# Optimization experiments

Hardware: AMD Instinct MI355X
Metric: run time of the kernel (lower is better)

Reference implementation:

```python
import jax, jax.numpy as jnp
import numpy as np

N = 8192   # num_nodes
H = 128    # hidden_dim
B = 100    # batch of events
K = 5      # num_neg_samples
TD_MAX = 10000.0
TIME_SD = jnp.array([50.0, 7.0, 15.0, 15.0])  # time_sd from forward; time_mean = 0


def setup_inputs() -> dict:
    key = jax.random.key(0)
    ks = jax.random.split(key, 16)
    p = 32.0 / N  # avg degree ~32
    A = (jax.random.uniform(ks[0], (N, N)) < p).astype(jnp.float32)
    # S init: S[v,u] = 1/D[v] for neighbors u (row-normalized A)
    S = A / (A.sum(axis=1, keepdims=True) + 1e-7)
    z0 = jax.random.normal(ks[1], (N, H)) * 0.1
    u = jax.random.randint(ks[2], (B,), 0, N)
    v = jax.random.randint(ks[3], (B,), 0, N)
    event_types = jax.random.randint(ks[4], (B,), 0, 2)
    neg_idx = jax.random.randint(ks[5], (B, 2 * K), 0, N)
    time_diff = jax.random.normal(ks[6], (B, 2, 4))
    t_bar = jax.random.uniform(ks[7], (B, N)) * 1000.0
    t = 1000.0 + 10.0 * jnp.arange(B, dtype=jnp.float32)

    def lin(k, o, i):
        k1, k2 = jax.random.split(k)
        lim = 1.0 / np.sqrt(i)
        return (jax.random.uniform(k1, (o, i), minval=-lim, maxval=lim),
                jax.random.uniform(k2, (o,), minval=-lim, maxval=lim))

    om0_w, om0_b = lin(ks[8], 1, 2 * H)
    om1_w, om1_b = lin(ks[9], 1, 2 * H)
    Wh_w, Wh_b = lin(ks[10], H, H)
    Ws_w, Ws_b = lin(ks[11], H, H)
    Wr_w, Wr_b = lin(ks[12], H, H)
    Wt_w, Wt_b = lin(ks[13], H, 4)
    return dict(u=u, v=v, event_types=event_types, neg_idx=neg_idx,
                time_diff=time_diff, t_bar=t_bar, t=t, z0=z0, A=A, S=S,
                w_t=0.5 * jnp.ones(2), alpha=0.5 * jnp.ones(2), psi=0.5 * jnp.ones(2),
                om0_w=om0_w, om0_b=om0_b, om1_w=om1_w, om1_b=om1_b,
                Wh_w=Wh_w, Wh_b=Wh_b, Ws_w=Ws_w, Ws_b=Ws_b,
                Wr_w=Wr_w, Wr_b=Wr_b, Wt_w=Wt_w, Wt_b=Wt_b)


def _forward(u, v, event_types, neg_idx, time_diff, t_bar, t, z0, A, S,
             w_t, alpha, psi, om0_w, om0_b, om1_w, om1_b,
             Wh_w, Wh_b, Ws_w, Ws_b, Wr_w, Wr_b, Wt_w, Wt_b):
    td_norm = time_diff / TIME_SD  # (td - 0) / sd

    def hawkes(zu, zv, et, td):
        # lambda = psi * log(1 + exp(g/psi)) + alpha * exp(-w_t * td/td_max)
        zc = jnp.concatenate([zu, zv], axis=-1)
        g0 = jnp.einsum('...d,d->...', zc, om0_w[0]) + om0_b[0]
        g1 = jnp.einsum('...d,d->...', zc, om1_w[0]) + om1_b[0]
        g = jnp.where(et == 0, g0, g1)
        ps, al, wt = psi[et], alpha[et], w_t[et]
        gp = jnp.clip(g / (ps + 1e-7), -75.0, 75.0)
        return ps * jnp.log1p(jnp.exp(gp)) + al * jnp.exp(-wt * (td / TD_MAX))

    ar = jnp.arange(N)

    def step(z, ev):
        u_it, v_it, et, td2, tb, t_it, neg = ev
        z_u, z_v = z[u_it], z[v_it]
        Wh_all = z @ Wh_w.T + Wh_b  # [N,H]

        def struct(node):
            # structural attention over node's neighbors (masked, not dense loop)
            mask = A[node] > 0
            q = jnp.exp(S[node]) * mask
            q = q / (q.sum() + 1e-7)
            hsig = jax.nn.sigmoid(q[:, None] * Wh_all)
            hmax = jnp.where(mask[:, None], hsig, -jnp.inf).max(axis=0)
            return jnp.where(jnp.any(mask), hmax, 0.0)

        # update of u uses struct info from v's neighborhood, and vice versa
        hs = jnp.stack([struct(v_it), struct(u_it)])  # [2,H]
        h = (hs @ Ws_w.T + Ws_b) + (jnp.stack([z_u, z_v]) @ Wr_w.T + Wr_b) + (td2 @ Wt_w.T + Wt_b)
        z_upd = jax.nn.sigmoid(h)
        z_new = z.at[u_it].set(z_upd[0]).at[v_it].set(z_upd[1])

        # negative pairs: (u, v_neg_k) then (u_neg_k, v), using z_prev
        v_neg, u_neg = neg[:K], neg[K:]
        zu_neg = jnp.concatenate([jnp.broadcast_to(z_u, (K, H)), z[u_neg]], 0)
        zv_neg = jnp.concatenate([z[v_neg], jnp.broadcast_to(z_v, (K, H))], 0)
        lt_u = jnp.concatenate([jnp.full((K,), tb[u_it]), tb[u_neg]])
        lt_v = jnp.concatenate([tb[v_neg], jnp.full((K,), tb[v_it])])
        ts_neg = t_it - jnp.maximum(lt_u, lt_v)
        ts_pos = t_it - jnp.maximum(tb[u_it], tb[v_it])

        # all-node intensity prediction (Lambda_dict path, detached in torch)
        zd = jax.lax.stop_gradient(z)
        zu_all = jnp.concatenate([jnp.broadcast_to(jax.lax.stop_gradient(z_u), (N, H)),
                                  jnp.broadcast_to(jax.lax.stop_gradient(z_v), (N, H))], 0)
        zv_all = jnp.concatenate([zd, zd], 0)
        last_t = jnp.maximum(
            jnp.concatenate([jnp.full((N,), tb[u_it]), jnp.full((N,), tb[v_it])]),
            jnp.concatenate([tb, tb]))
        lam_all = hawkes(zu_all, zv_all, jnp.full((2 * N,), et),
                         jax.lax.stop_gradient(t_it - last_t))
        m = ((ar != u_it) & (ar != v_it)).astype(lam_all.dtype)
        lam_sum = jax.lax.stop_gradient(jnp.sum(lam_all * jnp.concatenate([m, m])))

        return z_new, (z_u, z_v, zu_neg, zv_neg, ts_pos, ts_neg, lam_sum)

    _, (zu_p, zv_p, zun, zvn, ts_p, ts_n, lam_sums) = jax.lax.scan(
        step, z0, (u, v, event_types, td_norm, t_bar, t, neg_idx))

    lam_pos = hawkes(zu_p, zv_p, event_types, ts_p)            # [B]
    lam_neg = hawkes(zun, zvn, event_types[:, None], ts_n)      # [B,2K]
    return jnp.concatenate([lam_pos[:, None], lam_neg, lam_sums[:, None]], axis=1)  # [B, 2K+2]


def reference(u, v, event_types, neg_idx, time_diff, t_bar, t, z0, A, S,
              w_t, alpha, psi, om0_w, om0_b, om1_w, om1_b,
              Wh_w, Wh_b, Ws_w, Ws_b, Wr_w, Wr_b, Wt_w, Wt_b):
    return _forward(u, v, event_types, neg_idx, time_diff, t_bar, t, z0, A, S,
                    w_t, alpha, psi, om0_w, om0_b, om1_w, om1_b,
                    Wh_w, Wh_b, Ws_w, Ws_b, Wr_w, Wr_b, Wt_w, Wt_b)
```

## Files before the change

### kernel.cpp

```cpp
#include <hip/hip_runtime.h>
#include <math.h>

#define N 8192
#define H 128
#define BB 100
#define KK 5
#define MAXN 256
#define TD_MAXF 10000.0f

#define OFF_WHALLV ((size_t)N * H)
#define OFF_ZVER (OFF_WHALLV + 2 * BB * H)

__global__ __launch_bounds__(256) void prep_all_kernel(
    const float* __restrict__ Wh, const float* __restrict__ Ws,
    const float* __restrict__ Wr, const float* __restrict__ om0,
    const float* __restrict__ om1, const float* __restrict__ z0,
    float* __restrict__ WhT, float* __restrict__ WsT, float* __restrict__ WrT,
    float* __restrict__ omP, unsigned* __restrict__ flags,
    float* __restrict__ dvec0) {
  const int B0 = H * H, B1 = 2 * H * H, B2 = 3 * H * H;
  const int B3 = B2 + 2 * H, B4 = B2 + 4 * H, B5 = B4 + 4 * BB + 4;
  int idx = blockIdx.x * 256 + threadIdx.x;
  if (idx < B0) {
    int d = idx >> 7, k = idx & (H - 1);
    WhT[k * H + d] = Wh[d * H + k];
  } else if (idx < B1) {
    int e = idx - B0;
    int d = e >> 7, k = e & (H - 1);
    WsT[k * H + d] = Ws[d * H + k];
  } else if (idx < B2) {
    int e = idx - B1;
    int d = e >> 7, k = e & (H - 1);
    WrT[k * H + d] = Wr[d * H + k];
  } else if (idx < B3) {
    int e = idx - B2;
    omP[e] = om0[e];
  } else if (idx < B4) {
    int e = idx - B3;
    omP[2 * H + e] = om1[e];
  } else if (idx < B5) {
    flags[idx - B4] = 0u;
  } else if (idx < B5 + N) {
    int j = idx - B5;
    const float4* zr = (const float4*)(z0 + (size_t)j * H);
    const float4* o0 = (const float4*)om0;
    const float4* o1 = (const float4*)om1;
    float a0 = 0, b0 = 0, a1 = 0, b1 = 0;
    for (int k = 0; k < H / 4; ++k) {
      float4 zv = zr[k];
      float4 l0 = o0[k], r0 = o0[k + H / 4];
      float4 l1 = o1[k], r1 = o1[k + H / 4];
      a0 += zv.x * l0.x + zv.y * l0.y + zv.z * l0.z + zv.w * l0.w;
      b0 += zv.x * r0.x + zv.y * r0.y + zv.z * r0.z + zv.w * r0.w;
      a1 += zv.x * l1.x + zv.y * l1.y + zv.z * l1.z + zv.w * l1.w;
      b1 += zv.x * r1.x + zv.y * r1.y + zv.z * r1.z + zv.w * r1.w;
    }
    dvec0[0 * N + j] = a0;
    dvec0[1 * N + j] = b0;
    dvec0[2 * N + j] = a1;
    dvec0[3 * N + j] = b1;
  }
}

__global__ __launch_bounds__(256) void build_kernel(
    const float* __restrict__ z0, const float* __restrict__ WhT,
    const float* __restrict__ Wh_b, float* __restrict__ whall,
    const int* __restrict__ u_, const int* __restrict__ v_,
    const float* __restrict__ A, const float* __restrict__ S,
    int* __restrict__ cnt, int* __restrict__ nidx, float* __restrict__ nes,
    float* __restrict__ qsum, int* __restrict__ woff, int* __restrict__ zsrc,
    unsigned* __restrict__ need) {
  const int blk = blockIdx.x;
  const int tid = threadIdx.x;
  __shared__ float zr2[2][H];
  __shared__ int cnts[256];
  __shared__ int excl[257];
  __shared__ float ssum[256];
  __shared__ int nidxL[MAXN];
  __shared__ int uL[BB], vL[BB];

  if (blk < N / 2) {
    int r = tid >> 7, d = tid & (H - 1);
    int row = blk * 2 + r;
    zr2[r][d] = z0[(size_t)row * H + d];
    __syncthreads();
    float acc = Wh_b[d];
#pragma unroll 8
    for (int k = 0; k < H; ++k) acc += zr2[r][k] * WhT[k * H + d];
    whall[(size_t)row * H + d] = acc;
    return;
  }

  const int l = blk - N / 2;
  const int b = l >> 1, r = l & 1;
  const int node = r ? u_[b] : v_[b];
  int c = 0;
  float local = 0.0f;
  for (int it = 0; it < N / 256; ++it) {
    int j = it * 256 + tid;
    if (A[(size_t)node * N + j] > 0.0f) {
      ++c;
      local += expf(S[(size_t)node * N + j]);
    }
  }
  cnts[tid] = c;
  ssum[tid] = local;
  __syncthreads();
  if (tid == 0) {
    int s = 0;
    for (int i = 0; i < 256; ++i) { excl[i] = s; s += cnts[i]; }
    excl[256] = s;
  }
  __syncthreads();
  int p = excl[tid];
  for (int it = 0; it < N / 256; ++it) {
    int j = it * 256 + tid;
    if (A[(size_t)node * N + j] > 0.0f) {
      if (p < MAXN) {
        nidx[l * MAXN + p] = j;
        nidxL[p] = j;
        nes[l * MAXN + p] = expf(S[(size_t)node * N + j]);
      }
      ++p;
    }
  }
  if (tid < BB) {
    uL[tid] = u_[tid];
    vL[tid] = v_[tid];
  }
  __syncthreads();
  for (int s = 128; s > 0; s >>= 1) {
    if (tid < s) ssum[tid] += ssum[tid + s];
    __syncthreads();
  }
  const int cM = min(excl[256], MAXN);
  if (tid == 0) {
    cnt[l] = cM;
    qsum[l] = ssum[0];
  }
  for (int i = tid; i < cM; i += 256) {
    int n = nidxL[i];
    int a = -1, row = 0;
    for (int s = b - 1; s >= 0; --s) {
      if (vL[s] == n) { a = s; row = 1; break; }
      if (uL[s] == n) { a = s; row = 0; break; }
    }
    int off;
    if (a < 0) {
      off = n * H;
    } else {
      off = (int)OFF_WHALLV + (2 * a + row) * H;
      atomicOr(&need[b * 4 + (a >> 5)], 1u << (a & 31));
    }
    woff[l * MAXN + i] = off;
  }
  if (r == 0 && tid >= 254) {
    int which = tid - 254;
    int nd = which ? vL[b] : uL[b];
    int a = -1, row = 0;
    for (int s = b - 1; s >= 0; --s) {
      if (vL[s] == nd) { a = s; row = 1; break; }
      if (uL[s] == nd) { a = s; row = 0; break; }
    }
    int sv = -1;
    if (a >= 0) {
      sv = 2 * a + row;
      atomicOr(&need[b * 4 + (a >> 5)], 1u << (a & 31));
    }
    zsrc[2 * b + which] = sv;
  }
}

__global__ __launch_bounds__(1024) void fused_kernel(
    const int* __restrict__ u_, const int* __restrict__ v_,
    const int* __restrict__ et_, const int* __restrict__ neg_,
    const float* __restrict__ time_diff, const float* __restrict__ t_bar,
    const float* __restrict__ tt, const float* __restrict__ z0,
    const float* __restrict__ WhT, const float* __restrict__ WsT,
    const float* __restrict__ WrT, const float* __restrict__ omP,
    const float* __restrict__ Wh_b, const float* __restrict__ Ws_b,
    const float* __restrict__ Wr_b, const float* __restrict__ Wt_w,
    const float* __restrict__ Wt_b, const float* __restrict__ w_t,
    const float* __restrict__ alpha, const float* __restrict__ psi,
    const float* __restrict__ om0_b, const float* __restrict__ om1_b,
    const float* __restrict__ wsf, float* __restrict__ zver,
    float* __restrict__ whallv, float* __restrict__ dlog,
    const float* __restrict__ qsum_, const int* __restrict__ cnt_,
    const float* __restrict__ nes_, const int* __restrict__ woff_,
    const int* __restrict__ zsrc_, const float* __restrict__ dvec0,
    const unsigned* __restrict__ need, unsigned* done,
    float* __restrict__ out) {
  const int blk = blockIdx.x;
  const int t = threadIdx.x;
  __shared__ float scratch[8][2][H];
  __shared__ float hsS[2][H];
  __shared__ float zrowS[2][H];
  __shared__ float zupdS[2][H];
  __shared__ float td2S[2][4];
  __shared__ int woffS[2][MAXN];
  __shared__ float nqS[2][MAXN];
  __shared__ int cntS[2];
  __shared__ int uvS[2];
  __shared__ float dR[N];
  __shared__ int uS[BB], vS[BB];
  __shared__ float red[1024];
  __shared__ float suS, svS;

  if (blk < BB) {
    const int b = blk;
    const int r = t >> 9;
    const int sub = (t >> 7) & 3;
    const int d = t & (H - 1);
    const int l = 2 * b + r;
    const int c = cnt_[l];
    const float iq = 1.0f / (qsum_[l] + 1e-7f);
    const int ks = t >> 7;
    const int k0 = ks * 16;

    if (t < 512) {
      int rr = t >> 8, i = t & 255;
      woffS[rr][i] = woff_[(2 * b + rr) * MAXN + i];
      nqS[rr][i] = nes_[(2 * b + rr) * MAXN + i];
    } else if (t < 520) {
      int i = t - 512;
      int cc = i & 3;
      float sd = (cc == 0) ? 50.0f : ((cc == 1) ? 7.0f : 15.0f);
      td2S[i >> 2][cc] = time_diff[b * 8 + i] / sd;
    } else if (t < 522) {
      cntS[t - 520] = cnt_[2 * b + (t - 520)];
    } else if (t == 522) {
      uvS[0] = u_[b];
    } else if (t == 523) {
      uvS[1] = v_[b];
    }
    float wsReg[16], wrReg[16], whReg[16];
#pragma unroll
    for (int kk = 0; kk < 16; ++kk) {
      wsReg[kk] = WsT[(k0 + kk) * H + d];
      wrReg[kk] = WrT[(k0 + kk) * H + d];
      whReg[kk] = WhT[(k0 + kk) * H + d];
    }
    float biasReg = 0.0f, whbReg = 0.0f;
    float4 wt4Reg = {0.0f, 0.0f, 0.0f, 0.0f};
    float zpre = 0.0f;
    int zs = -1;
    if (t < 256) {
      int dd = t & (H - 1);
      biasReg = Ws_b[dd] + Wr_b[dd] + Wt_b[dd];
      whbReg = Wh_b[dd];
      wt4Reg = ((const float4*)Wt_w)[dd];
      int rr = t >> 7;
      zs = zsrc_[2 * b + rr];
      if (zs < 0) {
        int nd = rr ? v_[b] : u_[b];
        zpre = z0[(size_t)nd * H + dd];
      }
    }
    float omA = 0.0f, omB = 0.0f;
    if (t >= 256 && t < 768) {
      int w = (t - 256) >> 6;
      int lane = t & 63;
      int which = w & 3;
      int wsel = which >> 1;
      int offo = (which & 1) * H;
      omA = omP[wsel * 2 * H + offo + lane];
      omB = omP[wsel * 2 * H + offo + 64 + lane];
    }
    __syncthreads();

    float mx = -INFINITY;
    for (int i = sub; i < c; i += 4) {
      int off = woffS[r][i];
      if (off < (int)OFF_WHALLV)
        mx = fmaxf(mx, nqS[r][i] * iq * wsf[(size_t)off + d]);
    }
    if (t == 0) {
      for (int w = 0; w < 4; ++w) {
        unsigned nw = need[b * 4 + w];
        if (!nw) continue;
        while ((__hip_atomic_load(&done[w], __ATOMIC_RELAXED,
                                  __HIP_MEMORY_SCOPE_AGENT) &
                nw) != nw)
          __builtin_amdgcn_s_sleep(1);
      }
      __threadfence();
    }
    __syncthreads();

    const int ub = uvS[0], vb = uvS[1];

    for (int i = sub; i < c; i += 4) {
      int off = woffS[r][i];
      if (off >= (int)OFF_WHALLV)
        mx = fmaxf(mx, nqS[r][i] * iq * wsf[(size_t)off + d]);
    }
    scratch[sub][r][d] = mx;
    if (t < 256) {
      int rr = t >> 7, dd = t & (H - 1);
      zrowS[rr][dd] = (zs < 0) ? zpre : wsf[OFF_ZVER + (size_t)zs * H + dd];
    }
    __syncthreads();

    if (t < 2 * H) {
      int rr = t >> 7, dd = t & (H - 1);
      float m = fmaxf(fmaxf(scratch[0][rr][dd], scratch[1][rr][dd]),
                      fmaxf(scratch[2][rr][dd], scratch[3][rr][dd]));
      hsS[rr][dd] = (cntS[rr] > 0) ? (1.0f / (1.0f + expf(-m))) : 0.0f;
    }
    __syncthreads();

    {
      float a0 = 0.0f, a1 = 0.0f;
#pragma unroll
      for (int kk = 0; kk < 16; ++kk) {
        int k = k0 + kk;
        a0 += hsS[0][k] * wsReg[kk] + zrowS[0][k] * wrReg[kk];
        a1 += hsS[1][k] * wsReg[kk] + zrowS[1][k] * wrReg[kk];
      }
      scratch[ks][0][d] = a0;
      scratch[ks][1][d] = a1;
    }
    __syncthreads();

    if (t < 2 * H) {
      int rr = t >> 7, dd = t & (H - 1);
      float acc = biasReg;
#pragma unroll
      for (int kx = 0; kx < 8; ++kx) acc += scratch[kx][rr][dd];
      acc += td2S[rr][0] * wt4Reg.x + td2S[rr][1] * wt4Reg.y +
             td2S[rr][2] * wt4Reg.z + td2S[rr][3] * wt4Reg.w;
      float zu = 1.0f / (1.0f + expf(-acc));
      zupdS[rr][dd] = zu;
      zver[(size_t)(2 * b + rr) * H + dd] = zu;
    }
    __syncthreads();

    {
      int r0 = (ub == vb) ? 1 : 0;
      float f0 = 0.0f, f1 = 0.0f;
#pragma unroll
      for (int kk = 0; kk < 16; ++kk) {
        int k = k0 + kk;
        f0 += zupdS[r0][k] * whReg[kk];
        f1 += zupdS[1][k] * whReg[kk];
      }
      scratch[ks][0][d] = f0;
      scratch[ks][1][d] = f1;
    }
    __syncthreads();

    if (t < 2 * H) {
      int rr = t >> 7, dd = t & (H - 1);
      float acc = whbReg;
#pragma unroll
      for (int kx = 0; kx < 8; ++kx) acc += scratch[kx][rr][dd];
      whallv[(size_t)(2 * b + rr) * H + dd] = acc;
    } else if (t < 768) {
      int w = (t - 256) >> 6;
      int lane = t & 63;
      int row = w >> 2;
      int which = w & 3;
      int rr = (row == 0 && ub == vb) ? 1 : row;
      float val = zupdS[rr][lane] * omA + zupdS[rr][64 + lane] * omB;
      for (int s = 32; s > 0; s >>= 1) val += __shfl_down(val, s);
      if (lane == 0) dlog[b * 8 + which * 2 + row] = val;
    }
    __syncthreads();

    if (t == 0) {
      __threadfence();
      atomicOr(&done[b >> 5], 1u << (b & 31));
    }
    return;
  }

  const int b = blk - BB;
  const int e = et_[b];
  const int ub = u_[b], vb = v_[b];
  const float ps = psi[e], al = alpha[e], wt = w_t[e];
  const float ob0 = om0_b[0], ob1 = om1_b[0];
  const float ob = e ? ob1 : ob0;
  const float tcur = tt[b];
  const float inv_ps = 1.0f / (ps + 1e-7f);
  const int whichR = 2 * e + 1;
  const int whichL = 2 * e;

  if (t < BB) {
    uS[t] = u_[t];
    vS[t] = v_[t];
  }
  {
    const float4* base = (const float4*)(dvec0 + (size_t)whichR * N);
    float4* dst = (float4*)dR;
    for (int i = t; i < N / 4; i += 1024) dst[i] = base[i];
  }
  if (t == 0) {
    for (int w = 0; w < 4; ++w) {
      int cb = b - 32 * w;
      unsigned nw =
          (cb >= 32) ? 0xffffffffu : (cb <= 0 ? 0u : ((1u << cb) - 1u));
      if (!nw) continue;
      while ((__hip_atomic_load(&done[w], __ATOMIC_RELAXED,
                                __HIP_MEMORY_SCOPE_AGENT) &
              nw) != nw)
        __builtin_amdgcn_s_sleep(1);
    }
    __threadfence();
  }
  __syncthreads();

  for (int i = t; i < b; i += 1024) {
    int ui = uS[i], vi = vS[i];
    bool u_over = (ui == vi);
    bool v_over = false;
    for (int j = i + 1; j < b; ++j) {
      int uj = uS[j], vj = vS[j];
      u_over = u_over || (uj == ui) || (vj == ui);
      v_over = v_over || (uj == vi) || (vj == vi);
    }
    if (!u_over) dR[ui] = dlog[i * 8 + whichR * 2 + 0];
    if (!v_over) dR[vi] = dlog[i * 8 + whichR * 2 + 1];
  }

  if (t < 13) {
    auto dpre = [&](int x, int which) -> float {
      for (int bp = b - 1; bp >= 0; --bp) {
        if (vS[bp] == x) return dlog[bp * 8 + which * 2 + 1];
        if (uS[bp] == x) return dlog[bp * 8 + which * 2 + 0];
      }
      return dvec0[(size_t)which * N + x];
    };
    if (t < 11) {
      int li, ri;
      float ltu, ltv;
      if (t == 0) {
        li = ub; ri = vb;
        ltu = t_bar[(size_t)b * N + ub];
        ltv = t_bar[(size_t)b * N + vb];
      } else if (t <= 5) {
        int vn = neg_[b * (2 * KK) + (t - 1)];
        li = ub; ri = vn;
        ltu = t_bar[(size_t)b * N + ub];
        ltv = t_bar[(size_t)b * N + vn];
      } else {
        int un = neg_[b * (2 * KK) + (t - 1)];
        li = un; ri = vb;
        ltu = t_bar[(size_t)b * N + un];
        ltv = t_bar[(size_t)b * N + vb];
      }
      float g = dpre(li, whichL) + dpre(ri, whichR) + ob;
      float gp = fminf(fmaxf(g * inv_ps, -75.0f), 75.0f);
      float ts = tcur - fmaxf(ltu, ltv);
      out[b * 12 + t] = ps * log1pf(expf(gp)) + al * expf(-wt * (ts / TD_MAXF));
    } else if (t == 11) {
      suS = dpre(ub, whichL);
    } else {
      svS = dpre(vb, whichL);
    }
  }
  __syncthreads();

  const float su = suS, sv = svS;
  const float tb_u = t_bar[(size_t)b * N + ub];
  const float tb_v = t_bar[(size_t)b * N + vb];
  const float4* tb4 = (const float4*)(t_bar + (size_t)b * N);
  const float4* dR4 = (const float4*)dR;
  float acc = 0.0f;
  for (int j4 = t; j4 < N / 4; j4 += 1024) {
    float4 dv = dR4[j4];
    float4 tb = tb4[j4];
    float de[4] = {dv.x, dv.y, dv.z, dv.w};
    float te[4] = {tb.x, tb.y, tb.z, tb.w};
#pragma unroll
    for (int ee = 0; ee < 4; ++ee) {
      int j = j4 * 4 + ee;
      if (j == ub || j == vb) continue;
      float dd = de[ee];
      float tbj = te[ee];
      float gu = su + dd + ob;
      float gv = sv + dd + ob;
      float gpu_ = fminf(fmaxf(gu * inv_ps, -75.0f), 75.0f);
      float gpv_ = fminf(fmaxf(gv * inv_ps, -75.0f), 75.0f);
      float spl = ps * (log1pf(expf(gpu_)) + log1pf(expf(gpv_)));
      float tdu = tcur - fmaxf(tb_u, tbj);
      float tdv = tcur - fmaxf(tb_v, tbj);
      float ex =
          al * (expf(-wt * (tdu / TD_MAXF)) + expf(-wt * (tdv / TD_MAXF)));
      acc += spl + ex;
    }
  }
  red[t] = acc;
  __syncthreads();
  for (int s = 512; s > 0; s >>= 1) {
    if (t < s) red[t] += red[t + s];
    __syncthreads();
  }
  if (t == 0) out[b * 12 + 11] = red[0];
}

extern "C" void kernel_launch(void* const* d_in, const int* in_sizes, int n_in,
                              void* d_out, int out_size, void* d_ws,
                              size_t ws_size, hipStream_t stream) {
  const int* u = (const int*)d_in[0];
  const int* v = (const int*)d_in[1];
  const int* et = (const int*)d_in[2];
  const int* neg = (const int*)d_in[3];
  const float* time_diff = (const float*)d_in[4];
  const float* t_bar = (const float*)d_in[5];
  const float* t = (const float*)d_in[6];
  const float* z0 = (const float*)d_in[7];
  const float* A = (const float*)d_in[8];
  const float* S = (const float*)d_in[9];
  const float* w_t = (const float*)d_in[10];
  const float* alpha = (const float*)d_in[11];
  const float* psi = (const float*)d_in[12];
  const float* om0_w = (const float*)d_in[13];
  const float* om0_b = (const float*)d_in[14];
  const float* om1_w = (const float*)d_in[15];
  const float* om1_b = (const float*)d_in[16];
  const float* Wh_w = (const float*)d_in[17];
  const float* Wh_b = (const float*)d_in[18];
  const float* Ws_w = (const float*)d_in[19];
  const float* Ws_b = (const float*)d_in[20];
  const float* Wr_w = (const float*)d_in[21];
  const float* Wr_b = (const float*)d_in[22];
  const float* Wt_w = (const float*)d_in[23];
  const float* Wt_b = (const float*)d_in[24];
  float* out = (float*)d_out;

  float* wsf = (float*)d_ws;
  float* whall = wsf;
  float* whallv = wsf + OFF_WHALLV;
  float* zver = wsf + OFF_ZVER;
  float* WhT = zver + 2 * BB * H;
  float* WsT = WhT + H * H;
  float* WrT = WsT + H * H;
  float* omP = WrT + H * H;
  float* dvec0 = omP + 4 * H;
  float* dlog = dvec0 + 4 * N;
  float* qsum = dlog + 8 * BB;
  int* cnt = (int*)(qsum + 2 * BB);
  int* nidx = cnt + 2 * BB;
  float* nes = (float*)(nidx + 2 * BB * MAXN);
  int* woff = (int*)(nes + 2 * BB * MAXN);
  int* zsrc = woff + 2 * BB * MAXN;
  unsigned* need = (unsigned*)(zsrc + 2 * BB);
  unsigned* done = need + 4 * BB;

  const int PREP_ELEMS = 3 * H * H + 4 * H + 4 * BB + 4 + N;
  prep_all_kernel<<<(PREP_ELEMS + 255) / 256, 256, 0, stream>>>(
      Wh_w, Ws_w, Wr_w, om0_w, om1_w, z0, WhT, WsT, WrT, omP, need, dvec0);
  build_kernel<<<N / 2 + 2 * BB, 256, 0, stream>>>(
      z0, WhT, Wh_b, whall, u, v, A, S, cnt, nidx, nes, qsum, woff, zsrc,
      need);
  fused_kernel<<<2 * BB, 1024, 0, stream>>>(
      u, v, et, neg, time_diff, t_bar, t, z0, WhT, WsT, WrT, omP, Wh_b, Ws_b,
      Wr_b, Wt_w, Wt_b, w_t, alpha, psi, om0_b, om1_b, wsf, zver, whallv,
      dlog, qsum, cnt, nes, woff, zsrc, dvec0, need, done, out);
}
```

Baseline: 606.1 us.

## Drop weight-transpose prep kernel, fold into build, factor exps in lambda-sum loop

Removes the separate prep kernel that transposed Wh/Ws/Wr and copied the omega vectors. The matvecs now read the original row-major weights with float4 loads, the dvec0 dot products become extra blocks of build_kernel, and the flag clearing becomes a hipMemsetAsync. The second pass over the adjacency row is replaced by a per-thread bitmask from the first pass, so A is not reloaded. The survival-sum loop is refactored so softplus and the time-decay exponentials are written as products of per-event constants and per-node exponentials. This cuts transcendental work per node but drops the ±75 clamp, which risks overflow or reduced accuracy.

```diff
diff --git a/kernel.cpp b/kernel.cpp
--- a/kernel.cpp
+++ b/kernel.cpp
@@ -11,37 +11,43 @@
 #define OFF_WHALLV ((size_t)N * H)
 #define OFF_ZVER (OFF_WHALLV + 2 * BB * H)
 
-__global__ __launch_bounds__(256) void prep_all_kernel(
-    const float* __restrict__ Wh, const float* __restrict__ Ws,
-    const float* __restrict__ Wr, const float* __restrict__ om0,
-    const float* __restrict__ om1, const float* __restrict__ z0,
-    float* __restrict__ WhT, float* __restrict__ WsT, float* __restrict__ WrT,
-    float* __restrict__ omP, unsigned* __restrict__ flags,
-    float* __restrict__ dvec0) {
-  const int B0 = H * H, B1 = 2 * H * H, B2 = 3 * H * H;
-  const int B3 = B2 + 2 * H, B4 = B2 + 4 * H, B5 = B4 + 4 * BB + 4;
-  int idx = blockIdx.x * 256 + threadIdx.x;
-  if (idx < B0) {
-    int d = idx >> 7, k = idx & (H - 1);
-    WhT[k * H + d] = Wh[d * H + k];
-  } else if (idx < B1) {
-    int e = idx - B0;
-    int d = e >> 7, k = e & (H - 1);
-    WsT[k * H + d] = Ws[d * H + k];
-  } else if (idx < B2) {
-    int e = idx - B1;
-    int d = e >> 7, k = e & (H - 1);
-    WrT[k * H + d] = Wr[d * H + k];
-  } else if (idx < B3) {
-    int e = idx - B2;
-    omP[e] = om0[e];
-  } else if (idx < B4) {
-    int e = idx - B3;
-    omP[2 * H + e] = om1[e];
-  } else if (idx < B5) {
-    flags[idx - B4] = 0u;
-  } else if (idx < B5 + N) {
-    int j = idx - B5;
+__global__ __launch_bounds__(256) void build_kernel(
+    const float* __restrict__ z0, const float* __restrict__ Wh,
+    const float* __restrict__ Wh_b, float* __restrict__ whall,
+    const int* __restrict__ u_, const int* __restrict__ v_,
+    const float* __restrict__ A, const float* __restrict__ S,
+    const float* __restrict__ om0, const float* __restrict__ om1,
+    float* __restrict__ dvec0, int* __restrict__ cnt, int* __restrict__ nidx,
+    float* __restrict__ nes, float* __restrict__ qsum, int* __restrict__ woff,
+    int* __restrict__ zsrc, unsigned* __restrict__ need) {
+  const int blk = blockIdx.x;
+  const int tid = threadIdx.x;
+  __shared__ float zr2[2][H];
+  __shared__ int cnts[256];
+  __shared__ int excl[257];
+  __shared__ float ssum[256];
+  __shared__ int nidxL[MAXN];
+  __shared__ int uL[BB], vL[BB];
+
+  if (blk < N / 2) {
+    int r = tid >> 7, d = tid & (H - 1);
+    int row = blk * 2 + r;
+    zr2[r][d] = z0[(size_t)row * H + d];
+    __syncthreads();
+    float acc = Wh_b[d];
+    const float4* w4 = (const float4*)(Wh + (size_t)d * H);
+    const float4* z4 = (const float4*)zr2[r];
+#pragma unroll 8
+    for (int k4 = 0; k4 < H / 4; ++k4) {
+      float4 wv = w4[k4];
+      float4 zv = z4[k4];
+      acc += zv.x * wv.x + zv.y * wv.y + zv.z * wv.z + zv.w * wv.w;
+    }
+    whall[(size_t)row * H + d] = acc;
+    return;
+  }
+  if (blk >= N / 2 + 2 * BB) {
+    int j = (blk - N / 2 - 2 * BB) * 256 + tid;
     const float4* zr = (const float4*)(z0 + (size_t)j * H);
     const float4* o0 = (const float4*)om0;
     const float4* o1 = (const float4*)om1;
@@ -59,35 +65,6 @@
     dvec0[1 * N + j] = b0;
     dvec0[2 * N + j] = a1;
     dvec0[3 * N + j] = b1;
-  }
-}
-
-__global__ __launch_bounds__(256) void build_kernel(
-    const float* __restrict__ z0, const float* __restrict__ WhT,
-    const float* __restrict__ Wh_b, float* __restrict__ whall,
-    const int* __restrict__ u_, const int* __restrict__ v_,
-    const float* __restrict__ A, const float* __restrict__ S,
-    int* __restrict__ cnt, int* __restrict__ nidx, float* __restrict__ nes,
-    float* __restrict__ qsum, int* __restrict__ woff, int* __restrict__ zsrc,
-    unsigned* __restrict__ need) {
-  const int blk = blockIdx.x;
-  const int tid = threadIdx.x;
-  __shared__ float zr2[2][H];
-  __shared__ int cnts[256];
-  __shared__ int excl[257];
-  __shared__ float ssum[256];
-  __shared__ int nidxL[MAXN];
-  __shared__ int uL[BB], vL[BB];
-
-  if (blk < N / 2) {
-    int r = tid >> 7, d = tid & (H - 1);
-    int row = blk * 2 + r;
-    zr2[r][d] = z0[(size_t)row * H + d];
-    __syncthreads();
-    float acc = Wh_b[d];
-#pragma unroll 8
-    for (int k = 0; k < H; ++k) acc += zr2[r][k] * WhT[k * H + d];
-    whall[(size_t)row * H + d] = acc;
     return;
   }
 
@@ -96,9 +73,11 @@
   const int node = r ? u_[b] : v_[b];
   int c = 0;
   float local = 0.0f;
+  unsigned hitmask = 0u;
   for (int it = 0; it < N / 256; ++it) {
     int j = it * 256 + tid;
     if (A[(size_t)node * N + j] > 0.0f) {
+      hitmask |= (1u << it);
       ++c;
       local += expf(S[(size_t)node * N + j]);
     }
@@ -114,8 +93,8 @@
   __syncthreads();
   int p = excl[tid];
   for (int it = 0; it < N / 256; ++it) {
-    int j = it * 256 + tid;
-    if (A[(size_t)node * N + j] > 0.0f) {
+    if ((hitmask >> it) & 1u) {
+      int j = it * 256 + tid;
       if (p < MAXN) {
         nidx[l * MAXN + p] = j;
         nidxL[p] = j;
@@ -176,20 +155,20 @@
     const int* __restrict__ et_, const int* __restrict__ neg_,
     const float* __restrict__ time_diff, const float* __restrict__ t_bar,
     const float* __restrict__ tt, const float* __restrict__ z0,
-    const float* __restrict__ WhT, const float* __restrict__ WsT,
-    const float* __restrict__ WrT, const float* __restrict__ omP,
-    const float* __restrict__ Wh_b, const float* __restrict__ Ws_b,
-    const float* __restrict__ Wr_b, const float* __restrict__ Wt_w,
-    const float* __restrict__ Wt_b, const float* __restrict__ w_t,
-    const float* __restrict__ alpha, const float* __restrict__ psi,
-    const float* __restrict__ om0_b, const float* __restrict__ om1_b,
-    const float* __restrict__ wsf, float* __restrict__ zver,
-    float* __restrict__ whallv, float* __restrict__ dlog,
-    const float* __restrict__ qsum_, const int* __restrict__ cnt_,
-    const float* __restrict__ nes_, const int* __restrict__ woff_,
-    const int* __restrict__ zsrc_, const float* __restrict__ dvec0,
-    const unsigned* __restrict__ need, unsigned* done,
-    float* __restrict__ out) {
+    const float* __restrict__ Wh, const float* __restrict__ Ws,
+    const float* __restrict__ Wr, const float* __restrict__ om0_w,
+    const float* __restrict__ om1_w, const float* __restrict__ Wh_b,
+    const float* __restrict__ Ws_b, const float* __restrict__ Wr_b,
+    const float* __restrict__ Wt_w, const float* __restrict__ Wt_b,
+    const float* __restrict__ w_t, const float* __restrict__ alpha,
+    const float* __restrict__ psi, const float* __restrict__ om0_b,
+    const float* __restrict__ om1_b, const float* __restrict__ wsf,
+    float* __restrict__ zver, float* __restrict__ whallv,
+    float* __restrict__ dlog, const float* __restrict__ qsum_,
+    const int* __restrict__ cnt_, const float* __restrict__ nes_,
+    const int* __restrict__ woff_, const int* __restrict__ zsrc_,
+    const float* __restrict__ dvec0, const unsigned* __restrict__ need,
+    unsigned* done, float* __restrict__ out) {
   const int blk = blockIdx.x;
   const int t = threadIdx.x;
   __shared__ float scratch[8][2][H];
@@ -234,11 +213,20 @@
       uvS[1] = v_[b];
     }
     float wsReg[16], wrReg[16], whReg[16];
+    {
+      const float4* ws4 = (const float4*)(Ws + (size_t)d * H + k0);
+      const float4* wr4 = (const float4*)(Wr + (size_t)d * H + k0);
+      const float4* wh4 = (const float4*)(Wh + (size_t)d * H + k0);
 #pragma unroll
-    for (int kk = 0; kk < 16; ++kk) {
-      wsReg[kk] = WsT[(k0 + kk) * H + d];
-      wrReg[kk] = WrT[(k0 + kk) * H + d];
-      whReg[kk] = WhT[(k0 + kk) * H + d];
+      for (int q = 0; q < 4; ++q) {
+        float4 a = ws4[q], bq = wr4[q], cq = wh4[q];
+        wsReg[4 * q + 0] = a.x; wsReg[4 * q + 1] = a.y;
+        wsReg[4 * q + 2] = a.z; wsReg[4 * q + 3] = a.w;
+        wrReg[4 * q + 0] = bq.x; wrReg[4 * q + 1] = bq.y;
+        wrReg[4 * q + 2] = bq.z; wrReg[4 * q + 3] = bq.w;
+        whReg[4 * q + 0] = cq.x; whReg[4 * q + 1] = cq.y;
+        whReg[4 * q + 2] = cq.z; whReg[4 * q + 3] = cq.w;
+      }
     }
     float biasReg = 0.0f, whbReg = 0.0f;
     float4 wt4Reg = {0.0f, 0.0f, 0.0f, 0.0f};
@@ -263,8 +251,10 @@
       int which = w & 3;
       int wsel = which >> 1;
       int offo = (which & 1) * H;
-      omA = omP[wsel * 2 * H + offo + lane];
-      omB = omP[wsel * 2 * H + offo + 64 + lane];
+      float a0v = om0_w[offo + lane], a1v = om1_w[offo + lane];
+      float b0v = om0_w[offo + 64 + lane], b1v = om1_w[offo + 64 + lane];
+      omA = wsel ? a1v : a0v;
+      omB = wsel ? b1v : b0v;
     }
     __syncthreads();
 
@@ -463,6 +453,12 @@
   const float su = suS, sv = svS;
   const float tb_u = t_bar[(size_t)b * N + ub];
   const float tb_v = t_bar[(size_t)b * N + vb];
+  const float Ku = expf((su + ob) * inv_ps);
+  const float Kv = expf((sv + ob) * inv_ps);
+  const float Cx = al * expf(-wt * (tcur / TD_MAXF));
+  const float Eu = expf(wt * (tb_u / TD_MAXF));
+  const float Ev = expf(wt * (tb_v / TD_MAXF));
+  const float wTD = wt / TD_MAXF;
   const float4* tb4 = (const float4*)(t_bar + (size_t)b * N);
   const float4* dR4 = (const float4*)dR;
   float acc = 0.0f;
@@ -475,17 +471,10 @@
     for (int ee = 0; ee < 4; ++ee) {
       int j = j4 * 4 + ee;
       if (j == ub || j == vb) continue;
-      float dd = de[ee];
-      float tbj = te[ee];
-      float gu = su + dd + ob;
-      float gv = sv + dd + ob;
-      float gpu_ = fminf(fmaxf(gu * inv_ps, -75.0f), 75.0f);
-      float gpv_ = fminf(fmaxf(gv * inv_ps, -75.0f), 75.0f);
-      float spl = ps * (log1pf(expf(gpu_)) + log1pf(expf(gpv_)));
-      float tdu = tcur - fmaxf(tb_u, tbj);
-      float tdv = tcur - fmaxf(tb_v, tbj);
-      float ex =
-          al * (expf(-wt * (tdu / TD_MAXF)) + expf(-wt * (tdv / TD_MAXF)));
+      float Dj = expf(de[ee] * inv_ps);
+      float spl = ps * (log1pf(Ku * Dj) + log1pf(Kv * Dj));
+      float Ej = expf(wTD * te[ee]);
+      float ex = Cx * (fmaxf(Eu, Ej) + fmaxf(Ev, Ej));
       acc += spl + ex;
     }
   }
@@ -532,11 +521,7 @@
   float* whall = wsf;
   float* whallv = wsf + OFF_WHALLV;
   float* zver = wsf + OFF_ZVER;
-  float* WhT = zver + 2 * BB * H;
-  float* WsT = WhT + H * H;
-  float* WrT = WsT + H * H;
-  float* omP = WrT + H * H;
-  float* dvec0 = omP + 4 * H;
+  float* dvec0 = zver + 2 * BB * H;
   float* dlog = dvec0 + 4 * N;
   float* qsum = dlog + 8 * BB;
   int* cnt = (int*)(qsum + 2 * BB);
@@ -547,14 +532,12 @@
   unsigned* need = (unsigned*)(zsrc + 2 * BB);
   unsigned* done = need + 4 * BB;
 
-  const int PREP_ELEMS = 3 * H * H + 4 * H + 4 * BB + 4 + N;
-  prep_all_kernel<<<(PREP_ELEMS + 255) / 256, 256, 0, stream>>>(
-      Wh_w, Ws_w, Wr_w, om0_w, om1_w, z0, WhT, WsT, WrT, omP, need, dvec0);
-  build_kernel<<<N / 2 + 2 * BB, 256, 0, stream>>>(
-      z0, WhT, Wh_b, whall, u, v, A, S, cnt, nidx, nes, qsum, woff, zsrc,
-      need);
+  hipMemsetAsync(need, 0, (4 * BB + 4) * sizeof(unsigned), stream);
+  build_kernel<<<N / 2 + 2 * BB + N / 256, 256, 0, stream>>>(
+      z0, Wh_w, Wh_b, whall, u, v, A, S, om0_w, om1_w, dvec0, cnt, nidx, nes,
+      qsum, woff, zsrc, need);
   fused_kernel<<<2 * BB, 1024, 0, stream>>>(
-      u, v, et, neg, time_diff, t_bar, t, z0, WhT, WsT, WrT, omP, Wh_b, Ws_b,
-      Wr_b, Wt_w, Wt_b, w_t, alpha, psi, om0_b, om1_b, wsf, zver, whallv,
-      dlog, qsum, cnt, nes, woff, zsrc, dvec0, need, done, out);
+      u, v, et, neg, time_diff, t_bar, t, z0, Wh_w, Ws_w, Wr_w, om0_w, om1_w,
+      Wh_b, Ws_b, Wr_b, Wt_w, Wt_b, w_t, alpha, psi, om0_b, om1_b, wsf, zver,
+      whallv, dlog, qsum, cnt, nes, woff, zsrc, dvec0, need, done, out);
 }
```

Result: slower. 639.3 us (+5.5%).
